# Kernel optimization log

Measured on AMD Instinct MI355X. Metric: run time of the kernel, lower is better.

## Reference

```python
import jax, jax.numpy as jnp
import numpy as np

HEADS = 8
WINDOW = 25

def make_rel_pos_indices(ws=WINDOW):
    pos = np.arange(ws)
    gi, gj = np.meshgrid(pos, pos, indexing='ij')
    grid = np.stack([gi.reshape(-1), gj.reshape(-1)], axis=-1)  # (ws*ws, 2)
    rel = grid[:, None, :] - grid[None, :, :] + (ws - 1)        # (n, n, 2)
    return (rel[..., 0] * (2 * ws - 1) + rel[..., 1]).astype(np.int32)

def setup_inputs() -> dict:
    key = jax.random.key(0)
    k1, k2, k3, k4 = jax.random.split(key, 4)
    b, d, hw = 64, 256, WINDOW
    x = jax.random.normal(k1, (b, d, hw, hw), dtype=jnp.float32)
    w_qkv = jax.random.normal(k2, (d, 3 * d), dtype=jnp.float32) * 0.02
    w_out = jax.random.normal(k3, (d, d), dtype=jnp.float32) * 0.02
    bias_table = jax.random.normal(k4, ((2 * WINDOW - 1) ** 2, HEADS), dtype=jnp.float32) * 0.02
    rel_pos_indices = jnp.asarray(make_rel_pos_indices())
    return {"x": x, "w_qkv": w_qkv, "w_out": w_out,
            "bias_table": bias_table, "rel_pos_indices": rel_pos_indices}

def reference(x, w_qkv, w_out, bias_table, rel_pos_indices):
    b, d, H, W = x.shape
    heads = bias_table.shape[1]
    dh = d // heads
    scale = dh ** -0.5
    n = H * W
    # b d h w -> b n d
    xf = jnp.transpose(x, (0, 2, 3, 1)).reshape(b, n, d)
    qkv = xf @ w_qkv                                    # (b, n, 3d)
    q, k, v = jnp.split(qkv, 3, axis=-1)
    def to_heads(t):
        return jnp.transpose(t.reshape(b, n, heads, dh), (0, 2, 1, 3))  # b h n d
    q, k, v = to_heads(q) * scale, to_heads(k), to_heads(v)
    sim = jnp.einsum('bhid,bhjd->bhij', q, k)           # (b, h, n, n)
    bias = bias_table[rel_pos_indices]                  # (n, n, h)
    sim = sim + jnp.transpose(bias, (2, 0, 1))[None]
    attn = jax.nn.softmax(sim, axis=-1)
    out = jnp.einsum('bhij,bhjd->bhid', attn, v)        # (b, h, n, d)
    # b m (h w) d -> b h w (m d)
    out = jnp.transpose(out, (0, 2, 1, 3)).reshape(b, H, W, d)
    out = out @ w_out
    return jnp.transpose(out, (0, 3, 1, 2))             # b d h w
```

## Files before the change

### kernel.cpp

```cpp
#include <hip/hip_runtime.h>
#include <hip/hip_bf16.h>
#include <cstdint>
#include <cstddef>

#define NB 64
#define DD 256
#define NN 625
#define NP 640
#define NH 8
#define DH 32
#define N3 768
#define BSTR 640
#define LDK 72

typedef __attribute__((ext_vector_type(8))) short bf16x8;
typedef __attribute__((ext_vector_type(4))) float f32x4;
typedef unsigned long long ull;

__device__ __forceinline__ unsigned short f2bf(float f) {
    unsigned int x = __builtin_bit_cast(unsigned int, f);
    return (unsigned short)((x + 0x7fffu + ((x >> 16) & 1u)) >> 16);
}

__global__ __launch_bounds__(256)
void xT_kernel(const float* __restrict__ x, unsigned short* __restrict__ XT)
{
    __shared__ float T[64][65];
    const int b = blockIdx.z, n0 = blockIdx.x * 64, d0 = blockIdx.y * 64;
    const int tid = threadIdx.x;
    const float* xb = x + (size_t)b * DD * NN;
    #pragma unroll
    for (int r = 0; r < 16; ++r) {
        const int flat = r * 256 + tid;
        const int dd = flat >> 6, ii = flat & 63;
        const int n = n0 + ii;
        T[dd][ii] = (n < NN) ? xb[(size_t)(d0 + dd) * NN + n] : 0.f;
    }
    __syncthreads();
    #pragma unroll
    for (int r = 0; r < 16; ++r) {
        const int flat = r * 256 + tid;
        const int ii = flat >> 6, dd = flat & 63;
        XT[((size_t)b * NP + n0 + ii) * DD + d0 + dd] = f2bf(T[dd][ii]);
    }
}

__global__ __launch_bounds__(256)
void transpose_cast(const float* __restrict__ src, unsigned short* __restrict__ dst,
                    int R, int C)
{
    __shared__ float T[64][65];
    const int c0 = blockIdx.x * 64, r0 = blockIdx.y * 64;
    const int tid = threadIdx.x;
    #pragma unroll
    for (int r = 0; r < 16; ++r) {
        const int flat = r * 256 + tid;
        const int rr = flat >> 6, cc = flat & 63;
        T[rr][cc] = src[(size_t)(r0 + rr) * C + c0 + cc];
    }
    __syncthreads();
    #pragma unroll
    for (int r = 0; r < 16; ++r) {
        const int flat = r * 256 + tid;
        const int cc = flat >> 6, rr = flat & 63;
        dst[(size_t)(c0 + cc) * R + r0 + rr] = f2bf(T[rr][cc]);
    }
}

__global__ __launch_bounds__(256)
void biasT_kernel(const int* __restrict__ rel, const float* __restrict__ table,
                  float* __restrict__ biasT)
{
    __shared__ int sidx[64][65];
    const int i0 = blockIdx.x * 64, j0 = blockIdx.y * 64;
    const int tid = threadIdx.x;
    #pragma unroll
    for (int r = 0; r < 16; ++r) {
        const int flat = r * 256 + tid;
        const int ii = flat >> 6, jj = flat & 63;
        const int iG = i0 + ii, jG = j0 + jj;
        sidx[ii][jj] = (iG < NN && jG < NN) ? rel[(size_t)iG * NN + jG] : -1;
    }
    __syncthreads();
    for (int h = 0; h < NH; ++h) {
        #pragma unroll
        for (int r = 0; r < 16; ++r) {
            const int flat = r * 256 + tid;
            const int jj = flat >> 6, ii = flat & 63;
            const int iG = i0 + ii, jG = j0 + jj;
            const int idx = sidx[ii][jj];
            biasT[((size_t)h * BSTR + jG) * BSTR + iG] = (idx >= 0) ? table[idx * NH + h] : 0.f;
        }
    }
}

__global__ __launch_bounds__(256)
void qkv_mfma(const unsigned short* __restrict__ XT, const unsigned short* __restrict__ WT,
              unsigned short* __restrict__ Q, unsigned short* __restrict__ K,
              unsigned short* __restrict__ V)
{
    __shared__ unsigned short As[128][LDK];
    __shared__ unsigned short Bs[128][LDK];

    const int b = blockIdx.z, i0 = blockIdx.x * 128, j0 = blockIdx.y * 128;
    const int tid = threadIdx.x, lane = tid & 63, w = tid >> 6;
    const int lo = lane & 15, hi = lane >> 4;
    const int wr = w >> 1, wc = w & 1;

    const unsigned short* Abase = XT + (size_t)b * NP * DD;
    const unsigned short* Bbase = WT;

    const int srow = tid >> 3;
    const int sc   = (tid & 7) * 8;

    f32x4 acc[4][4];
    #pragma unroll
    for (int a = 0; a < 4; ++a)
        #pragma unroll
        for (int t = 0; t < 4; ++t) acc[a][t] = (f32x4){0.f, 0.f, 0.f, 0.f};

    for (int k0 = 0; k0 < DD; k0 += 64) {
        #pragma unroll
        for (int p = 0; p < 4; ++p) {
            const int row = p * 32 + srow;
            *(bf16x8*)&As[row][sc] = *(const bf16x8*)&Abase[(size_t)(i0 + row) * DD + k0 + sc];
            *(bf16x8*)&Bs[row][sc] = *(const bf16x8*)&Bbase[(size_t)(j0 + row) * DD + k0 + sc];
        }
        __syncthreads();
        #pragma unroll
        for (int kk = 0; kk < 64; kk += 32) {
            bf16x8 af[4], bfr[4];
            #pragma unroll
            for (int a = 0; a < 4; ++a)
                af[a] = *(const bf16x8*)&As[wr * 64 + a * 16 + lo][kk + 8 * hi];
            #pragma unroll
            for (int t = 0; t < 4; ++t)
                bfr[t] = *(const bf16x8*)&Bs[wc * 64 + t * 16 + lo][kk + 8 * hi];
            #pragma unroll
            for (int a = 0; a < 4; ++a)
                #pragma unroll
                for (int t = 0; t < 4; ++t)
                    acc[a][t] = __builtin_amdgcn_mfma_f32_16x16x32_bf16(af[a], bfr[t], acc[a][t], 0, 0, 0);
        }
        __syncthreads();
    }

    #pragma unroll
    for (int t = 0; t < 4; ++t) {
        const int j  = j0 + wc * 64 + t * 16 + lo;
        const int tt = j >> 8;
        const int h  = (j & 255) >> 5;
        const int cb = j & 31;
        unsigned short* dst = (tt == 0) ? Q : (tt == 1) ? K : V;
        const float mul = (tt == 0) ? 0.17677669529663687f : 1.f;
        #pragma unroll
        for (int a = 0; a < 4; ++a) {
            #pragma unroll
            for (int r = 0; r < 4; ++r) {
                const int i = i0 + wr * 64 + a * 16 + 4 * hi + r;
                if (i < NN)
                    dst[(((size_t)b * NH + h) * NN + i) * DH + cb] = f2bf(acc[a][t][r] * mul);
            }
        }
    }
}

__global__ __launch_bounds__(256)
void attn_kernel(const unsigned short* __restrict__ Q,
                 const unsigned short* __restrict__ K,
                 const unsigned short* __restrict__ V,
                 const float* __restrict__ biasT, unsigned short* __restrict__ AO)
{
    __shared__ unsigned short Ks[32][40];
    __shared__ unsigned short Vt[32][40];
    __shared__ unsigned short Pl[4][16][40];

    const int b  = blockIdx.z;
    const int h  = blockIdx.y;
    const int i0 = blockIdx.x * 64;
    const int tid  = threadIdx.x;
    const int lane = tid & 63;
    const int w    = tid >> 6;
    const int lo   = lane & 15;
    const int hi   = lane >> 4;

    const size_t hoff = ((size_t)b * NH + h) * (size_t)NN * DH;

    const int iq  = i0 + w * 16 + lo;
    const int iqc = (iq < NN) ? iq : (NN - 1);
    const bf16x8 qf = *(const bf16x8*)&Q[hoff + (size_t)iqc * DH + 8 * hi];

    const float* bh = biasT + (size_t)h * BSTR * BSTR;
    const int ibase = i0 + w * 16 + 4 * hi;

    f32x4 acc0 = {0.f, 0.f, 0.f, 0.f};
    f32x4 acc1 = {0.f, 0.f, 0.f, 0.f};
    float lsum[4] = {0.f, 0.f, 0.f, 0.f};

    for (int j0c = 0; j0c < NN; j0c += 32) {
        {
            const int j  = tid >> 3;
            const int c0 = (tid & 7) * 4;
            const int jj = j0c + j;
            ull kd = 0;
            if (jj < NN) kd = *(const ull*)&K[hoff + (size_t)jj * DH + c0];
            *(ull*)&Ks[j][c0] = kd;

            const int jv  = tid & 31;
            const int cv0 = ((tid >> 5) & 7) * 4;
            const int jjv = j0c + jv;
            ushort4 vd = make_ushort4(0, 0, 0, 0);
            if (jjv < NN) vd = *(const ushort4*)&V[hoff + (size_t)jjv * DH + cv0];
            Vt[cv0 + 0][jv] = vd.x; Vt[cv0 + 1][jv] = vd.y;
            Vt[cv0 + 2][jv] = vd.z; Vt[cv0 + 3][jv] = vd.w;
        }
        __syncthreads();

        const float* bb = bh + (size_t)(j0c + lo) * BSTR + ibase;
        const f32x4 b0 = *(const f32x4*)bb;
        const f32x4 b1 = *(const f32x4*)(bb + (size_t)16 * BSTR);

        const bf16x8 kf0 = *(const bf16x8*)&Ks[lo][8 * hi];
        const bf16x8 kf1 = *(const bf16x8*)&Ks[16 + lo][8 * hi];
        const f32x4 s0 = __builtin_amdgcn_mfma_f32_16x16x32_bf16(qf, kf0, b0, 0, 0, 0);
        const f32x4 s1 = __builtin_amdgcn_mfma_f32_16x16x32_bf16(qf, kf1, b1, 0, 0, 0);

        const bool v0 = (j0c + lo) < NN;
        const bool v1 = (j0c + 16 + lo) < NN;
        float p0[4], p1[4];
        #pragma unroll
        for (int r = 0; r < 4; ++r) {
            p0[r] = v0 ? __expf(s0[r]) : 0.f;
            p1[r] = v1 ? __expf(s1[r]) : 0.f;
            lsum[r] += p0[r] + p1[r];
        }
        #pragma unroll
        for (int r = 0; r < 4; ++r) {
            Pl[w][4 * hi + r][lo]      = f2bf(p0[r]);
            Pl[w][4 * hi + r][16 + lo] = f2bf(p1[r]);
        }
        const bf16x8 pf  = *(const bf16x8*)&Pl[w][lo][8 * hi];
        const bf16x8 vf0 = *(const bf16x8*)&Vt[lo][8 * hi];
        const bf16x8 vf1 = *(const bf16x8*)&Vt[16 + lo][8 * hi];
        acc0 = __builtin_amdgcn_mfma_f32_16x16x32_bf16(pf, vf0, acc0, 0, 0, 0);
        acc1 = __builtin_amdgcn_mfma_f32_16x16x32_bf16(pf, vf1, acc1, 0, 0, 0);

        __syncthreads();
    }

    #pragma unroll
    for (int off = 1; off < 16; off <<= 1)
        #pragma unroll
        for (int r = 0; r < 4; ++r)
            lsum[r] += __shfl_xor(lsum[r], off, 64);

    #pragma unroll
    for (int r = 0; r < 4; ++r) {
        const int i = ibase + r;
        if (i < NN) {
            const float inv = 1.f / lsum[r];
            unsigned short* dst = AO + ((size_t)b * NP + i) * DD + h * DH;
            dst[lo]      = f2bf(acc0[r] * inv);
            dst[16 + lo] = f2bf(acc1[r] * inv);
        }
    }
}

__global__ __launch_bounds__(256)
void outproj_mfma(const unsigned short* __restrict__ AO, const unsigned short* __restrict__ WoT,
                  float* __restrict__ out)
{
    __shared__ unsigned short As[128][LDK];
    __shared__ unsigned short Bs[128][LDK];

    const int b = blockIdx.z, i0 = blockIdx.x * 128, j0 = blockIdx.y * 128;
    const int tid = threadIdx.x, lane = tid & 63, w = tid >> 6;
    const int lo = lane & 15, hi = lane >> 4;
    const int wr = w >> 1, wc = w & 1;

    const unsigned short* Abase = AO + (size_t)b * NP * DD;

    const int srow = tid >> 3;
    const int sc   = (tid & 7) * 8;

    f32x4 acc[4][4];
    #pragma unroll
    for (int a = 0; a < 4; ++a)
        #pragma unroll
        for (int t = 0; t < 4; ++t) acc[a][t] = (f32x4){0.f, 0.f, 0.f, 0.f};

    for (int k0 = 0; k0 < DD; k0 += 64) {
        #pragma unroll
        for (int p = 0; p < 4; ++p) {
            const int row = p * 32 + srow;
            *(bf16x8*)&As[row][sc] = *(const bf16x8*)&Abase[(size_t)(i0 + row) * DD + k0 + sc];
            *(bf16x8*)&Bs[row][sc] = *(const bf16x8*)&WoT[(size_t)(j0 + row) * DD + k0 + sc];
        }
        __syncthreads();
        #pragma unroll
        for (int kk = 0; kk < 64; kk += 32) {
            bf16x8 af[4], bfr[4];
            #pragma unroll
            for (int a = 0; a < 4; ++a)
                af[a] = *(const bf16x8*)&As[wr * 64 + a * 16 + lo][kk + 8 * hi];
            #pragma unroll
            for (int t = 0; t < 4; ++t)
                bfr[t] = *(const bf16x8*)&Bs[wc * 64 + t * 16 + lo][kk + 8 * hi];
            #pragma unroll
            for (int a = 0; a < 4; ++a)
                #pragma unroll
                for (int t = 0; t < 4; ++t)
                    acc[a][t] = __builtin_amdgcn_mfma_f32_16x16x32_bf16(af[a], bfr[t], acc[a][t], 0, 0, 0);
        }
        __syncthreads();
    }

    #pragma unroll
    for (int t = 0; t < 4; ++t) {
        const int j = j0 + wc * 64 + t * 16 + lo;
        float* dst = out + ((size_t)b * DD + j) * NN;
        #pragma unroll
        for (int a = 0; a < 4; ++a) {
            #pragma unroll
            for (int r = 0; r < 4; ++r) {
                const int i = i0 + wr * 64 + a * 16 + 4 * hi + r;
                if (i < NN) dst[i] = acc[a][t][r];
            }
        }
    }
}

extern "C" void kernel_launch(void* const* d_in, const int* in_sizes, int n_in,
                              void* d_out, int out_size, void* d_ws, size_t ws_size,
                              hipStream_t stream)
{
    (void)in_sizes; (void)n_in; (void)out_size; (void)ws_size;
    const float* x     = (const float*)d_in[0];
    const float* w_qkv = (const float*)d_in[1];
    const float* w_out = (const float*)d_in[2];
    const float* table = (const float*)d_in[3];
    const int*   rel   = (const int*)d_in[4];
    float* out = (float*)d_out;

    unsigned short* ws16 = (unsigned short*)d_ws;
    const size_t szQ  = (size_t)NB * NH * NN * DH;
    const size_t szXT = (size_t)NB * NP * DD;
    unsigned short* Q   = ws16;
    unsigned short* K   = Q + szQ;
    unsigned short* V   = K + szQ;
    unsigned short* XT  = V + szQ;
    unsigned short* WT  = XT + szXT;
    unsigned short* WoT = WT + (size_t)N3 * DD;
    unsigned short* AO  = WoT + (size_t)DD * DD;
    float* BT = (float*)(AO + szXT);

    xT_kernel     <<<dim3(10, 4, NB), 256, 0, stream>>>(x, XT);
    transpose_cast<<<dim3(12, 4, 1),  256, 0, stream>>>(w_qkv, WT, DD, N3);
    transpose_cast<<<dim3(4, 4, 1),   256, 0, stream>>>(w_out, WoT, DD, DD);
    biasT_kernel  <<<dim3(10, 10, 1), 256, 0, stream>>>(rel, table, BT);
    qkv_mfma      <<<dim3(5, 6, NB),  256, 0, stream>>>(XT, WT, Q, K, V);
    attn_kernel   <<<dim3(10, NH, NB), 256, 0, stream>>>(Q, K, V, BT, AO);
    outproj_mfma  <<<dim3(5, 2, NB),  256, 0, stream>>>(AO, WoT, out);
}
```

Measured before the change: 272.2 us.

## Double-buffer K/V tiles and prefetch bias in attention kernel

The attention loop now processes 64 keys per iteration, split into two 32-key MFMA substeps. K, V and bias values for the next chunk are loaded into registers and written into a second shared-memory buffer while the current chunk is computed. This halves the number of barriers per key and hides global-load latency behind the MFMA and exp work. In exchange it uses more registers and LDS, which can lower occupancy. The loop bound is hard-coded to 10 chunks.

```diff
diff --git a/kernel.cpp b/kernel.cpp
--- a/kernel.cpp
+++ b/kernel.cpp
@@ -12,6 +12,8 @@
 #define N3 768
 #define BSTR 640
 #define LDK 72
+#define KVB 64
+#define VSTR 72
 
 typedef __attribute__((ext_vector_type(8))) short bf16x8;
 typedef __attribute__((ext_vector_type(4))) float f32x4;
@@ -171,8 +173,8 @@
                  const unsigned short* __restrict__ V,
                  const float* __restrict__ biasT, unsigned short* __restrict__ AO)
 {
-    __shared__ unsigned short Ks[32][40];
-    __shared__ unsigned short Vt[32][40];
+    __shared__ unsigned short Ks[2][KVB][40];
+    __shared__ unsigned short Vt[2][DH][VSTR];
     __shared__ unsigned short Pl[4][16][40];
 
     const int b  = blockIdx.z;
@@ -193,58 +195,79 @@
     const float* bh = biasT + (size_t)h * BSTR * BSTR;
     const int ibase = i0 + w * 16 + 4 * hi;
 
+    const int srow = tid & 63;
+    const int sc   = (tid >> 6) * 8;
+
     f32x4 acc0 = {0.f, 0.f, 0.f, 0.f};
     f32x4 acc1 = {0.f, 0.f, 0.f, 0.f};
     float lsum[4] = {0.f, 0.f, 0.f, 0.f};
 
-    for (int j0c = 0; j0c < NN; j0c += 32) {
-        {
-            const int j  = tid >> 3;
-            const int c0 = (tid & 7) * 4;
-            const int jj = j0c + j;
-            ull kd = 0;
-            if (jj < NN) kd = *(const ull*)&K[hoff + (size_t)jj * DH + c0];
-            *(ull*)&Ks[j][c0] = kd;
-
-            const int jv  = tid & 31;
-            const int cv0 = ((tid >> 5) & 7) * 4;
-            const int jjv = j0c + jv;
-            ushort4 vd = make_ushort4(0, 0, 0, 0);
-            if (jjv < NN) vd = *(const ushort4*)&V[hoff + (size_t)jjv * DH + cv0];
-            Vt[cv0 + 0][jv] = vd.x; Vt[cv0 + 1][jv] = vd.y;
-            Vt[cv0 + 2][jv] = vd.z; Vt[cv0 + 3][jv] = vd.w;
-        }
-        __syncthreads();
-
-        const float* bb = bh + (size_t)(j0c + lo) * BSTR + ibase;
-        const f32x4 b0 = *(const f32x4*)bb;
-        const f32x4 b1 = *(const f32x4*)(bb + (size_t)16 * BSTR);
-
-        const bf16x8 kf0 = *(const bf16x8*)&Ks[lo][8 * hi];
-        const bf16x8 kf1 = *(const bf16x8*)&Ks[16 + lo][8 * hi];
-        const f32x4 s0 = __builtin_amdgcn_mfma_f32_16x16x32_bf16(qf, kf0, b0, 0, 0, 0);
-        const f32x4 s1 = __builtin_amdgcn_mfma_f32_16x16x32_bf16(qf, kf1, b1, 0, 0, 0);
-
-        const bool v0 = (j0c + lo) < NN;
-        const bool v1 = (j0c + 16 + lo) < NN;
-        float p0[4], p1[4];
-        #pragma unroll
-        for (int r = 0; r < 4; ++r) {
-            p0[r] = v0 ? __expf(s0[r]) : 0.f;
-            p1[r] = v1 ? __expf(s1[r]) : 0.f;
-            lsum[r] += p0[r] + p1[r];
-        }
-        #pragma unroll
-        for (int r = 0; r < 4; ++r) {
-            Pl[w][4 * hi + r][lo]      = f2bf(p0[r]);
-            Pl[w][4 * hi + r][16 + lo] = f2bf(p1[r]);
-        }
-        const bf16x8 pf  = *(const bf16x8*)&Pl[w][lo][8 * hi];
-        const bf16x8 vf0 = *(const bf16x8*)&Vt[lo][8 * hi];
-        const bf16x8 vf1 = *(const bf16x8*)&Vt[16 + lo][8 * hi];
-        acc0 = __builtin_amdgcn_mfma_f32_16x16x32_bf16(pf, vf0, acc0, 0, 0, 0);
-        acc1 = __builtin_amdgcn_mfma_f32_16x16x32_bf16(pf, vf1, acc1, 0, 0, 0);
-
+    {
+        bf16x8 k0 = {0,0,0,0,0,0,0,0}, v0 = {0,0,0,0,0,0,0,0};
+        if (srow < NN) {
+            k0 = *(const bf16x8*)&K[hoff + (size_t)srow * DH + sc];
+            v0 = *(const bf16x8*)&V[hoff + (size_t)srow * DH + sc];
+        }
+        *(bf16x8*)&Ks[0][srow][sc] = k0;
+        #pragma unroll
+        for (int e = 0; e < 8; ++e) Vt[0][sc + e][srow] = (unsigned short)v0[e];
+    }
+    f32x4 bc[4];
+    #pragma unroll
+    for (int r = 0; r < 4; ++r)
+        bc[r] = *(const f32x4*)&bh[(size_t)(r * 16 + lo) * BSTR + ibase];
+    __syncthreads();
+
+    for (int t = 0; t < 10; ++t) {
+        const int cur = t & 1;
+        bf16x8 kn = {0,0,0,0,0,0,0,0}, vn = {0,0,0,0,0,0,0,0};
+        f32x4 bn[4];
+        const int jn = (t + 1) * KVB;
+        if (t < 9) {
+            const int jr = jn + srow;
+            if (jr < NN) {
+                kn = *(const bf16x8*)&K[hoff + (size_t)jr * DH + sc];
+                vn = *(const bf16x8*)&V[hoff + (size_t)jr * DH + sc];
+            }
+            #pragma unroll
+            for (int r = 0; r < 4; ++r)
+                bn[r] = *(const f32x4*)&bh[(size_t)(jn + r * 16 + lo) * BSTR + ibase];
+        }
+        #pragma unroll
+        for (int s = 0; s < 2; ++s) {
+            const int js = s * 32;
+            const int jbase = t * KVB + js;
+            const bf16x8 kf0 = *(const bf16x8*)&Ks[cur][js + lo][8 * hi];
+            const bf16x8 kf1 = *(const bf16x8*)&Ks[cur][js + 16 + lo][8 * hi];
+            const f32x4 s0 = __builtin_amdgcn_mfma_f32_16x16x32_bf16(qf, kf0, bc[2*s+0], 0, 0, 0);
+            const f32x4 s1 = __builtin_amdgcn_mfma_f32_16x16x32_bf16(qf, kf1, bc[2*s+1], 0, 0, 0);
+            const bool v0 = (jbase + lo) < NN;
+            const bool v1 = (jbase + 16 + lo) < NN;
+            float p0[4], p1[4];
+            #pragma unroll
+            for (int r = 0; r < 4; ++r) {
+                p0[r] = v0 ? __expf(s0[r]) : 0.f;
+                p1[r] = v1 ? __expf(s1[r]) : 0.f;
+                lsum[r] += p0[r] + p1[r];
+            }
+            #pragma unroll
+            for (int r = 0; r < 4; ++r) {
+                Pl[w][4 * hi + r][lo]      = f2bf(p0[r]);
+                Pl[w][4 * hi + r][16 + lo] = f2bf(p1[r]);
+            }
+            const bf16x8 pf  = *(const bf16x8*)&Pl[w][lo][8 * hi];
+            const bf16x8 vf0 = *(const bf16x8*)&Vt[cur][lo][js + 8 * hi];
+            const bf16x8 vf1 = *(const bf16x8*)&Vt[cur][16 + lo][js + 8 * hi];
+            acc0 = __builtin_amdgcn_mfma_f32_16x16x32_bf16(pf, vf0, acc0, 0, 0, 0);
+            acc1 = __builtin_amdgcn_mfma_f32_16x16x32_bf16(pf, vf1, acc1, 0, 0, 0);
+        }
+        if (t < 9) {
+            *(bf16x8*)&Ks[cur ^ 1][srow][sc] = kn;
+            #pragma unroll
+            for (int e = 0; e < 8; ++e) Vt[cur ^ 1][sc + e][srow] = (unsigned short)vn[e];
+            #pragma unroll
+            for (int r = 0; r < 4; ++r) bc[r] = bn[r];
+        }
         __syncthreads();
     }
 
```

After: 255.6 us. 1.06x faster.

## Restructure attention: full V tile in LDS, transposed S, register-shuffled P

Applied to the files above, without the earlier changes.

The attention kernel now stages the whole transposed V for a head into swizzled shared memory once and drops the per-chunk K/V staging and its two barriers per iteration. K fragments are read straight from global memory. S is computed transposed (K×Q) so the bias can be read row-contiguous from a non-transposed bias layout. P is packed with v_cvt_pk_bf16 and redistributed through lane shuffles instead of an LDS round trip. The bias precompute kernel is changed to write the non-transposed layout, and launch bounds request 4 blocks per CU. The trade is about 40KB of LDS per block, which may limit occupancy, plus more shuffle instructions per iteration.

```diff
diff --git a/kernel.cpp b/kernel.cpp
--- a/kernel.cpp
+++ b/kernel.cpp
@@ -15,11 +15,16 @@
 
 typedef __attribute__((ext_vector_type(8))) short bf16x8;
 typedef __attribute__((ext_vector_type(4))) float f32x4;
-typedef unsigned long long ull;
+typedef unsigned int u32;
 
 __device__ __forceinline__ unsigned short f2bf(float f) {
-    unsigned int x = __builtin_bit_cast(unsigned int, f);
+    u32 x = __builtin_bit_cast(u32, f);
     return (unsigned short)((x + 0x7fffu + ((x >> 16) & 1u)) >> 16);
+}
+__device__ __forceinline__ u32 cvt_pk_bf16(float a, float b) {
+    u32 r;
+    asm("v_cvt_pk_bf16_f32 %0, %1, %2" : "=v"(r) : "v"(a), "v"(b));
+    return r;
 }
 
 __global__ __launch_bounds__(256)
@@ -68,10 +73,9 @@
 }
 
 __global__ __launch_bounds__(256)
-void biasT_kernel(const int* __restrict__ rel, const float* __restrict__ table,
-                  float* __restrict__ biasT)
-{
-    __shared__ int sidx[64][65];
+void bias2_kernel(const int* __restrict__ rel, const float* __restrict__ table,
+                  float* __restrict__ bias2)
+{
     const int i0 = blockIdx.x * 64, j0 = blockIdx.y * 64;
     const int tid = threadIdx.x;
     #pragma unroll
@@ -79,18 +83,10 @@
         const int flat = r * 256 + tid;
         const int ii = flat >> 6, jj = flat & 63;
         const int iG = i0 + ii, jG = j0 + jj;
-        sidx[ii][jj] = (iG < NN && jG < NN) ? rel[(size_t)iG * NN + jG] : -1;
-    }
-    __syncthreads();
-    for (int h = 0; h < NH; ++h) {
-        #pragma unroll
-        for (int r = 0; r < 16; ++r) {
-            const int flat = r * 256 + tid;
-            const int jj = flat >> 6, ii = flat & 63;
-            const int iG = i0 + ii, jG = j0 + jj;
-            const int idx = sidx[ii][jj];
-            biasT[((size_t)h * BSTR + jG) * BSTR + iG] = (idx >= 0) ? table[idx * NH + h] : 0.f;
-        }
+        const int idx = (iG < NN && jG < NN) ? rel[(size_t)iG * NN + jG] : -1;
+        #pragma unroll
+        for (int h = 0; h < NH; ++h)
+            bias2[((size_t)h * BSTR + iG) * BSTR + jG] = (idx >= 0) ? table[idx * NH + h] : 0.f;
     }
 }
 
@@ -165,15 +161,13 @@
     }
 }
 
-__global__ __launch_bounds__(256)
+__global__ __launch_bounds__(256, 4)
 void attn_kernel(const unsigned short* __restrict__ Q,
                  const unsigned short* __restrict__ K,
                  const unsigned short* __restrict__ V,
-                 const float* __restrict__ biasT, unsigned short* __restrict__ AO)
-{
-    __shared__ unsigned short Ks[32][40];
-    __shared__ unsigned short Vt[32][40];
-    __shared__ unsigned short Pl[4][16][40];
+                 const float* __restrict__ bias2, unsigned short* __restrict__ AO)
+{
+    __shared__ unsigned short Vt[DH][640];
 
     const int b  = blockIdx.z;
     const int h  = blockIdx.y;
@@ -186,82 +180,87 @@
 
     const size_t hoff = ((size_t)b * NH + h) * (size_t)NN * DH;
 
+    {
+        const int jr = tid & 63;
+        const int sc = (tid >> 6) * 8;
+        for (int it = 0; it < 10; ++it) {
+            const int j = it * 64 + jr;
+            bf16x8 vv = {0, 0, 0, 0, 0, 0, 0, 0};
+            if (j < NN) vv = *(const bf16x8*)&V[hoff + (size_t)j * DH + sc];
+            #pragma unroll
+            for (int e = 0; e < 8; ++e)
+                Vt[sc + e][j ^ (((sc + e) & 7) << 3)] = (unsigned short)vv[e];
+        }
+    }
+
     const int iq  = i0 + w * 16 + lo;
     const int iqc = (iq < NN) ? iq : (NN - 1);
     const bf16x8 qf = *(const bf16x8*)&Q[hoff + (size_t)iqc * DH + 8 * hi];
 
-    const float* bh = biasT + (size_t)h * BSTR * BSTR;
-    const int ibase = i0 + w * 16 + 4 * hi;
+    const float* bb = bias2 + ((size_t)h * BSTR + iq) * BSTR;
+
+    __syncthreads();
 
     f32x4 acc0 = {0.f, 0.f, 0.f, 0.f};
     f32x4 acc1 = {0.f, 0.f, 0.f, 0.f};
-    float lsum[4] = {0.f, 0.f, 0.f, 0.f};
-
-    for (int j0c = 0; j0c < NN; j0c += 32) {
-        {
-            const int j  = tid >> 3;
-            const int c0 = (tid & 7) * 4;
-            const int jj = j0c + j;
-            ull kd = 0;
-            if (jj < NN) kd = *(const ull*)&K[hoff + (size_t)jj * DH + c0];
-            *(ull*)&Ks[j][c0] = kd;
-
-            const int jv  = tid & 31;
-            const int cv0 = ((tid >> 5) & 7) * 4;
-            const int jjv = j0c + jv;
-            ushort4 vd = make_ushort4(0, 0, 0, 0);
-            if (jjv < NN) vd = *(const ushort4*)&V[hoff + (size_t)jjv * DH + cv0];
-            Vt[cv0 + 0][jv] = vd.x; Vt[cv0 + 1][jv] = vd.y;
-            Vt[cv0 + 2][jv] = vd.z; Vt[cv0 + 3][jv] = vd.w;
-        }
-        __syncthreads();
-
-        const float* bb = bh + (size_t)(j0c + lo) * BSTR + ibase;
-        const f32x4 b0 = *(const f32x4*)bb;
-        const f32x4 b1 = *(const f32x4*)(bb + (size_t)16 * BSTR);
-
-        const bf16x8 kf0 = *(const bf16x8*)&Ks[lo][8 * hi];
-        const bf16x8 kf1 = *(const bf16x8*)&Ks[16 + lo][8 * hi];
-        const f32x4 s0 = __builtin_amdgcn_mfma_f32_16x16x32_bf16(qf, kf0, b0, 0, 0, 0);
-        const f32x4 s1 = __builtin_amdgcn_mfma_f32_16x16x32_bf16(qf, kf1, b1, 0, 0, 0);
-
-        const bool v0 = (j0c + lo) < NN;
-        const bool v1 = (j0c + 16 + lo) < NN;
+    float lsum = 0.f;
+
+    const int src0 = lo + ((hi & 1) << 5);
+    const int src1 = src0 + 16;
+    const bool selA = (hi < 2);
+    const int swz = (lo & 7) << 3;
+
+    #pragma unroll 2
+    for (int ss = 0; ss < 20; ++ss) {
+        const int jb = ss * 32;
+        const int kr0 = jb + lo, kr1 = jb + 16 + lo;
+        const bf16x8 kf0 = *(const bf16x8*)&K[hoff + (size_t)(kr0 < NN ? kr0 : NN - 1) * DH + 8 * hi];
+        const bf16x8 kf1 = *(const bf16x8*)&K[hoff + (size_t)(kr1 < NN ? kr1 : NN - 1) * DH + 8 * hi];
+        const f32x4 b0 = *(const f32x4*)&bb[jb + 4 * hi];
+        const f32x4 b1 = *(const f32x4*)&bb[jb + 16 + 4 * hi];
+        const f32x4 s0 = __builtin_amdgcn_mfma_f32_16x16x32_bf16(kf0, qf, b0, 0, 0, 0);
+        const f32x4 s1 = __builtin_amdgcn_mfma_f32_16x16x32_bf16(kf1, qf, b1, 0, 0, 0);
+
         float p0[4], p1[4];
         #pragma unroll
         for (int r = 0; r < 4; ++r) {
-            p0[r] = v0 ? __expf(s0[r]) : 0.f;
-            p1[r] = v1 ? __expf(s1[r]) : 0.f;
-            lsum[r] += p0[r] + p1[r];
-        }
-        #pragma unroll
-        for (int r = 0; r < 4; ++r) {
-            Pl[w][4 * hi + r][lo]      = f2bf(p0[r]);
-            Pl[w][4 * hi + r][16 + lo] = f2bf(p1[r]);
-        }
-        const bf16x8 pf  = *(const bf16x8*)&Pl[w][lo][8 * hi];
-        const bf16x8 vf0 = *(const bf16x8*)&Vt[lo][8 * hi];
-        const bf16x8 vf1 = *(const bf16x8*)&Vt[16 + lo][8 * hi];
-        acc0 = __builtin_amdgcn_mfma_f32_16x16x32_bf16(pf, vf0, acc0, 0, 0, 0);
-        acc1 = __builtin_amdgcn_mfma_f32_16x16x32_bf16(pf, vf1, acc1, 0, 0, 0);
-
-        __syncthreads();
-    }
-
-    #pragma unroll
-    for (int off = 1; off < 16; off <<= 1)
-        #pragma unroll
-        for (int r = 0; r < 4; ++r)
-            lsum[r] += __shfl_xor(lsum[r], off, 64);
+            const bool m0 = (jb + 4 * hi + r) < NN;
+            const bool m1 = (jb + 16 + 4 * hi + r) < NN;
+            p0[r] = m0 ? __expf(s0[r]) : 0.f;
+            p1[r] = m1 ? __expf(s1[r]) : 0.f;
+            lsum += p0[r] + p1[r];
+        }
+        const u32 A0 = cvt_pk_bf16(p0[0], p0[1]);
+        const u32 A1 = cvt_pk_bf16(p0[2], p0[3]);
+        const u32 B0 = cvt_pk_bf16(p1[0], p1[1]);
+        const u32 B1 = cvt_pk_bf16(p1[2], p1[3]);
+        const u32 a0 = __shfl(A0, src0, 64), c0 = __shfl(B0, src0, 64);
+        const u32 a1 = __shfl(A1, src0, 64), c1 = __shfl(B1, src0, 64);
+        const u32 a2 = __shfl(A0, src1, 64), c2 = __shfl(B0, src1, 64);
+        const u32 a3 = __shfl(A1, src1, 64), c3 = __shfl(B1, src1, 64);
+        union { u32 u[4]; bf16x8 v; } P;
+        P.u[0] = selA ? a0 : c0;
+        P.u[1] = selA ? a1 : c1;
+        P.u[2] = selA ? a2 : c2;
+        P.u[3] = selA ? a3 : c3;
+        const bf16x8 vf0 = *(const bf16x8*)&Vt[lo][(jb + 8 * hi) ^ swz];
+        const bf16x8 vf1 = *(const bf16x8*)&Vt[16 + lo][(jb + 8 * hi) ^ swz];
+        acc0 = __builtin_amdgcn_mfma_f32_16x16x32_bf16(P.v, vf0, acc0, 0, 0, 0);
+        acc1 = __builtin_amdgcn_mfma_f32_16x16x32_bf16(P.v, vf1, acc1, 0, 0, 0);
+    }
+
+    lsum += __shfl_xor(lsum, 16, 64);
+    lsum += __shfl_xor(lsum, 32, 64);
+    const float inv = 1.f / lsum;
 
     #pragma unroll
     for (int r = 0; r < 4; ++r) {
-        const int i = ibase + r;
+        const int i = i0 + w * 16 + 4 * hi + r;
+        const float invr = __shfl(inv, 4 * hi + r, 64);
         if (i < NN) {
-            const float inv = 1.f / lsum[r];
             unsigned short* dst = AO + ((size_t)b * NP + i) * DD + h * DH;
-            dst[lo]      = f2bf(acc0[r] * inv);
-            dst[16 + lo] = f2bf(acc1[r] * inv);
+            dst[lo]      = f2bf(acc0[r] * invr);
+            dst[16 + lo] = f2bf(acc1[r] * invr);
         }
     }
 }
@@ -352,13 +351,13 @@
     unsigned short* WT  = XT + szXT;
     unsigned short* WoT = WT + (size_t)N3 * DD;
     unsigned short* AO  = WoT + (size_t)DD * DD;
-    float* BT = (float*)(AO + szXT);
+    float* B2 = (float*)(AO + szXT);
 
     xT_kernel     <<<dim3(10, 4, NB), 256, 0, stream>>>(x, XT);
     transpose_cast<<<dim3(12, 4, 1),  256, 0, stream>>>(w_qkv, WT, DD, N3);
     transpose_cast<<<dim3(4, 4, 1),   256, 0, stream>>>(w_out, WoT, DD, DD);
-    biasT_kernel  <<<dim3(10, 10, 1), 256, 0, stream>>>(rel, table, BT);
+    bias2_kernel  <<<dim3(10, 10, 1), 256, 0, stream>>>(rel, table, B2);
     qkv_mfma      <<<dim3(5, 6, NB),  256, 0, stream>>>(XT, WT, Q, K, V);
-    attn_kernel   <<<dim3(10, NH, NB), 256, 0, stream>>>(Q, K, V, BT, AO);
+    attn_kernel   <<<dim3(10, NH, NB), 256, 0, stream>>>(Q, K, V, B2, AO);
     outproj_mfma  <<<dim3(5, 2, NB),  256, 0, stream>>>(AO, WoT, out);
 }
```

New measurement: 278.6 us. 1.02x slower.
